# Performance work log

Hardware: AMD Instinct MI355X
Metric: run time of the kernel (lower is better)

Reference implementation:

```python
import jax, jax.numpy as jnp
import numpy as np

VOC, D, CPR, RELS = 2048, 128, 128, 7
B, DEPTH = 512, 4  # complete binary trees: 2**DEPTH leaves per tree


def setup_inputs() -> dict:
    key = jax.random.key(0)
    ks = jax.random.split(key, 13)
    s = lambda k, shape, fan: jax.random.normal(k, shape, jnp.float32) / np.sqrt(fan)
    return {
        "leaf_ids": jax.random.randint(ks[0], (B, 2, 2 ** DEPTH), 0, VOC),
        "Wv": s(ks[1], (D, VOC), VOC), "bv": jnp.zeros((D,), jnp.float32),
        "Wcps": s(ks[2], (D, 2 * D), 2 * D), "bcps": jnp.zeros((D,), jnp.float32),
        "Wcpst": s(ks[3], (D, D * D), D * D), "bcpst": jnp.zeros((D,), jnp.float32),
        "Wcpr": s(ks[4], (CPR, 2 * D), 2 * D), "bcpr": jnp.zeros((CPR,), jnp.float32),
        "Wcprt": s(ks[5], (CPR, D * D), D * D), "bcprt": jnp.zeros((CPR,), jnp.float32),
        "Wsm": s(ks[6], (RELS, CPR), CPR), "bsm": jnp.zeros((RELS,), jnp.float32),
    }


def reference(leaf_ids, Wv, bv, Wcps, bcps, Wcpst, bcpst, Wcpr, bcpr, Wcprt, bcprt, Wsm, bsm):
    d = Wv.shape[0]
    # leaf embedding: voc(one_hot(idx)) == Wv[:, idx] + bv  -> [B, 2, L, d]
    h = jnp.take(Wv.T, leaf_ids, axis=0) + bv
    # batched level-by-level tree composition (complete binary trees)
    while h.shape[2] > 1:
        l, r = h[:, :, 0::2, :], h[:, :, 1::2, :]
        lin = jnp.concatenate([l, r], axis=-1) @ Wcps.T + bcps
        kron = (l[..., :, None] * r[..., None, :]).reshape(l.shape[:-1] + (d * d,))
        h = jnp.tanh(lin + kron @ Wcpst.T + bcpst)
    lc, rc = h[:, 0, 0, :], h[:, 1, 0, :]  # [B, d] each
    cpr = jnp.concatenate([lc, rc], axis=-1) @ Wcpr.T + bcpr
    kron = (lc[:, :, None] * rc[:, None, :]).reshape(lc.shape[0], d * d)
    act = jax.nn.leaky_relu(cpr + kron @ Wcprt.T + bcprt, 0.01)
    logits = act @ Wsm.T + bsm
    return jax.nn.log_softmax(logits, axis=-1)  # [B, RELS]
```

## Files before the change

kernel.cpp:

```cpp
#include <hip/hip_runtime.h>
#include <hip/hip_bf16.h>
#include <hip/hip_fp16.h>

#define DD    128
#define VOCAB 2048
#define NRELS 7
#define NWF   (130 * 16384)

typedef _Float16 f16;
typedef __attribute__((ext_vector_type(8))) _Float16 f16x8;
typedef __attribute__((ext_vector_type(4))) float    f32x4;

__device__ __forceinline__ float lde(const void* p, size_t i, int bf) {
    if (bf) return (float)((const __hip_bfloat16*)p)[i];
    return ((const float*)p)[i];
}

__device__ __forceinline__ int detect_bf(const unsigned short* wv) {
    int sane = 0;
    #pragma unroll
    for (int i = 0; i < 64; ++i) {
        unsigned e = (wv[i] >> 7) & 0xFFu;
        sane += (e >= 90u && e <= 160u) ? 1 : 0;
    }
    return sane == 64;
}

__global__ void prep_all(const void* Wv, const void* bv,
                         const void* Wcps, const void* bcps,
                         const void* Wcpst, const void* bcpst,
                         const void* Wcpr, const void* bcpr,
                         const void* Wcprt, const void* bcprt,
                         const void* Wsm, const void* bsm,
                         f16* __restrict__ WvT, f16* __restrict__ Wext, f16* __restrict__ Wfin,
                         float* __restrict__ bias_lvl, float* __restrict__ bias_fin,
                         float* __restrict__ Wsm_f, float* __restrict__ bsm_f)
{
    const int bf = detect_bf((const unsigned short*)Wv);
    const int b = blockIdx.x;
    const int tid = threadIdx.x;

    if (b < 64) {
        __shared__ float tile[64][65];
        int vt = b >> 1, dt = b & 1;
        int tx = tid & 63, ty = tid >> 6;
        for (int yy = ty; yy < 64; yy += 4)
            tile[yy][tx] = lde(Wv, (size_t)(dt * 64 + yy) * VOCAB + vt * 64 + tx, bf);
        __syncthreads();
        for (int yy = ty; yy < 64; yy += 4) {
            int v = vt * 64 + yy, d = dt * 64 + tx;
            __builtin_nontemporal_store((f16)(tile[tx][yy] + lde(bv, d, bf)),
                                        &WvT[(size_t)v * DD + d]);
        }
        return;
    }
    if (b >= 2144) {
        if (tid < 128)      bias_lvl[tid] = lde(bcps, tid, bf) + lde(bcpst, tid, bf);
        else if (tid < 256) bias_fin[tid - 128] = lde(bcpr, tid - 128, bf) + lde(bcprt, tid - 128, bf);
        for (int o = tid; o < NRELS * DD; o += 256) Wsm_f[o] = lde(Wsm, o, bf);
        if (tid < NRELS) bsm_f[tid] = lde(bsm, tid, bf);
        return;
    }
    const int bb    = b - 64;
    const int which = bb / 1040;
    const int rem   = bb - which * 1040;
    const int i     = rem >> 3;
    const int n8    = rem & 7;
    const void* Wt = which ? (const void*)Wcprt : (const void*)Wcpst;
    const void* Ws = which ? (const void*)Wcpr  : (const void*)Wcps;
    f16* dst = which ? Wfin : Wext;

    __shared__ float tile[16 * 129];
    #pragma unroll
    for (int it = 0; it < 8; ++it) {
        int idx = it * 256 + tid;
        int rr = idx >> 7, c = idx & 127;
        float v = (i < 128) ? lde(Wt, (size_t)(n8 * 16 + rr) * 16384 + (size_t)i * 128 + c, bf)
                            : lde(Ws, (size_t)(n8 * 16 + rr) * 256 + (size_t)(i - 128) * 128 + c, bf);
        tile[rr * 129 + c] = v;
    }
    __syncthreads();
    f16* out = dst + (size_t)(i * 8 + n8) * 2048;
    #pragma unroll
    for (int it = 0; it < 8; ++it) {
        int o = it * 256 + tid;
        int t = o >> 9, ln = (o >> 3) & 63, e = o & 7;
        __builtin_nontemporal_store((f16)tile[(ln & 15) * 129 + t * 32 + ((ln >> 4) << 3) + e],
                                    &out[o]);
    }
}

template<int BI, int NW>
__launch_bounds__(NW * 64, 2)
__global__ void gemm_kernel(const f16* __restrict__ hin, const int* __restrict__ ids,
                            const f16* __restrict__ Wf,
                            f16* __restrict__ part, int Mrows, int S)
{
    __shared__ f16 Wb[4][8192];

    const int tid  = threadIdx.x;
    const int lane = tid & 63;
    const int wv   = tid >> 6;
    const int b    = blockIdx.x;
    const int nh   = (b >> 2) & 1;
    const int r    = ((b >> 3) << 2) | (b & 3);
    const int mb   = r / S;
    const int s    = r - mb * S;
    const int m0   = mb * (NW * 64);
    const int i0   = s * BI;
    const bool tail = (s == 1 || s == 2);
    const int itail = (s == 1) ? 128 : 129;

    const int mrow = lane & 15;
    const int q    = lane >> 4;
    const int wm   = wv * 64;

    f16x8 rf[4][4];
    int rowL[4];
    #pragma unroll
    for (int mt = 0; mt < 4; ++mt) {
        int p = m0 + wm + mt * 16 + mrow;
        int row = ids ? ids[2 * p + 1] : 2 * p + 1;
        rowL[mt] = ids ? ids[2 * p] : 2 * p;
        #pragma unroll
        for (int t = 0; t < 4; ++t)
            rf[mt][t] = *(const f16x8*)&hin[(size_t)row * DD + t * 32 + q * 8];
    }

    f16 lw[4][BI];
    #pragma unroll
    for (int mt = 0; mt < 4; ++mt) {
        const f16* src = &hin[(size_t)rowL[mt] * DD + i0];
        if constexpr (BI == 16) { *(f16x8*)&lw[mt][0] = *(const f16x8*)src;
                                  *(f16x8*)&lw[mt][8] = *(const f16x8*)(src + 8); }
        else if constexpr (BI == 8) { *(f16x8*)&lw[mt][0] = *(const f16x8*)src; }
        else if constexpr (BI == 4) { *(unsigned long long*)&lw[mt][0] = *(const unsigned long long*)src; }
        else if constexpr (BI == 2) { *(unsigned int*)&lw[mt][0] = *(const unsigned int*)src; }
        else { lw[mt][0] = src[0]; }
    }

    auto stage = [&](int i, int slot) {
        const f16* g = Wf + (size_t)i * 16384 + nh * 8192;
        #pragma unroll
        for (int k = 0; k < 16 / NW; ++k) {
            int j = k * NW + wv;
            const f16* gg = g + (size_t)(j * 64 + lane) * 8;
            f16* l = &Wb[slot][(size_t)(j * 64) * 8];
            __builtin_amdgcn_global_load_lds(
                (const __attribute__((address_space(1))) unsigned int*)gg,
                (__attribute__((address_space(3))) unsigned int*)l, 16, 0, 0);
        }
    };

    stage(i0, 0);
    if (BI > 1)       stage(i0 + 1, 1);
    else if (tail)    stage(itail, 1);
    __syncthreads();

    f32x4 acc[4][4] = {};

#define TSTEP(T, SLOT, KRON, LBV)                                                       \
    {                                                                                   \
        f16x8 wc[4];                                                                    \
        _Pragma("unroll")                                                               \
        for (int nt = 0; nt < 4; ++nt)                                                  \
            wc[nt] = *(const f16x8*)&Wb[SLOT][nt * 2048 + (T) * 512 + lane * 8];        \
        _Pragma("unroll")                                                               \
        for (int mt = 0; mt < 4; ++mt) {                                                \
            f16x8 a = (KRON) ? (LBV[mt] * rf[mt][T]) : rf[mt][T];                       \
            _Pragma("unroll")                                                           \
            for (int nt = 0; nt < 4; ++nt)                                              \
                acc[mt][nt] = __builtin_amdgcn_mfma_f32_16x16x32_f16(a, wc[nt], acc[mt][nt], 0, 0, 0); \
        }                                                                               \
    }

    #pragma unroll
    for (int ii = 0; ii < BI; ++ii) {
        if (ii + 2 < BI)                 stage(i0 + ii + 2, (ii + 2) & 3);
        else if (ii + 2 == BI && tail)   stage(itail, BI & 3);
        f16x8 lb[4];
        #pragma unroll
        for (int mt = 0; mt < 4; ++mt) {
            f16 v = lw[mt][ii];
            #pragma unroll
            for (int e = 0; e < 8; ++e) lb[mt][e] = v;
        }
        TSTEP(0, ii & 3, true, lb); TSTEP(1, ii & 3, true, lb);
        TSTEP(2, ii & 3, true, lb); TSTEP(3, ii & 3, true, lb);
        if (ii & 1) __syncthreads();
    }

    if (tail) {
        const int slot = (BI > 1) ? (BI & 3) : 1;
        if (s == 1) {
            #pragma unroll
            for (int mt = 0; mt < 4; ++mt)
                #pragma unroll
                for (int t = 0; t < 4; ++t)
                    rf[mt][t] = *(const f16x8*)&hin[(size_t)rowL[mt] * DD + t * 32 + q * 8];
        }
        f16x8 dummy[4];
        TSTEP(0, slot, false, dummy); TSTEP(1, slot, false, dummy);
        TSTEP(2, slot, false, dummy); TSTEP(3, slot, false, dummy);
    }
#undef TSTEP

    f16* pb = part + ((size_t)s * Mrows + m0) * DD + nh * 64;
    #pragma unroll
    for (int mt = 0; mt < 4; ++mt)
        #pragma unroll
        for (int nt = 0; nt < 4; ++nt) {
            int colg = nt * 16 + mrow;
            #pragma unroll
            for (int rr = 0; rr < 4; ++rr) {
                int rowl = wm + mt * 16 + q * 4 + rr;
                pb[(size_t)rowl * DD + colg] = (f16)acc[mt][nt][rr];
            }
        }
}

__global__ void epi_level(const f16* __restrict__ part, const float* __restrict__ bias,
                          f16* __restrict__ hout, int Mrows, int S)
{
    int idx = (blockIdx.x * 256 + threadIdx.x) * 8;
    size_t stride = (size_t)Mrows * DD;
    float sum[8] = {};
    for (int s2 = 0; s2 < S; ++s2) {
        f16x8 v = *(const f16x8*)&part[(size_t)s2 * stride + idx];
        #pragma unroll
        for (int e = 0; e < 8; ++e) sum[e] += (float)v[e];
    }
    int n = idx & 127;
    f16x8 o;
    #pragma unroll
    for (int e = 0; e < 8; ++e) o[e] = (f16)tanhf(sum[e] + bias[n + e]);
    *(f16x8*)&hout[idx] = o;
}

__global__ void fin_epi(const f16* __restrict__ part, const float* __restrict__ bias,
                        const float* __restrict__ Wsm_f, const float* __restrict__ bsm_f,
                        const unsigned short* __restrict__ wv_raw, void* __restrict__ outp, int S)
{
    int lane = threadIdx.x & 63;
    int wv = threadIdx.x >> 6;
    int p = blockIdx.x * 4 + wv;
    size_t stride = (size_t)512 * DD;
    const f16* base = part + (size_t)p * DD;
    float a0 = 0.f, a1 = 0.f;
    for (int s2 = 0; s2 < S; ++s2) {
        a0 += (float)base[(size_t)s2 * stride + lane];
        a1 += (float)base[(size_t)s2 * stride + 64 + lane];
    }
    a0 += bias[lane];      a1 += bias[64 + lane];
    a0 = (a0 > 0.f) ? a0 : 0.01f * a0;
    a1 = (a1 > 0.f) ? a1 : 0.01f * a1;
    float lg[NRELS];
    #pragma unroll
    for (int r = 0; r < NRELS; ++r) {
        float pr = a0 * Wsm_f[r * DD + lane] + a1 * Wsm_f[r * DD + 64 + lane];
        #pragma unroll
        for (int d = 1; d < 64; d <<= 1) pr += __shfl_xor(pr, d, 64);
        lg[r] = pr + bsm_f[r];
    }
    float mx = lg[0];
    #pragma unroll
    for (int r = 1; r < NRELS; ++r) mx = fmaxf(mx, lg[r]);
    float se = 0.f;
    #pragma unroll
    for (int r = 0; r < NRELS; ++r) se += expf(lg[r] - mx);
    float lse = logf(se) + mx;
    if (lane < NRELS) {
        float v = lg[lane] - lse;
        if (detect_bf(wv_raw)) ((__hip_bfloat16*)outp)[p * NRELS + lane] = __float2bfloat16(v);
        else                   ((float*)outp)[p * NRELS + lane] = v;
    }
}

extern "C" void kernel_launch(void* const* d_in, const int* in_sizes, int n_in,
                              void* d_out, int out_size, void* d_ws, size_t ws_size,
                              hipStream_t stream)
{
    const int* ids = (const int*)d_in[0];

    char* ws = (char*)d_ws;
    f16*   part     = (f16*)ws;
    f16*   h1       = (f16*)(ws + ((size_t)32 << 20));
    f16*   h2       = (f16*)(ws + ((size_t)34 << 20));
    f16*   h3       = (f16*)(ws + ((size_t)35 << 20));
    f16*   h4       = (f16*)(ws + ((size_t)35 << 20) + (512 << 10));
    f16*   WvT      = (f16*)(ws + ((size_t)36 << 20));
    f16*   Wext     = (f16*)(ws + ((size_t)36 << 20) + (512 << 10));
    f16*   Wfin     = Wext + (size_t)NWF;
    float* bias_lvl = (float*)(Wfin + (size_t)NWF);
    float* bias_fin = bias_lvl + 128;
    float* Wsm_f    = bias_fin + 128;
    float* bsm_f    = Wsm_f + NRELS * DD;

    if (ws_size < ((size_t)48 << 20)) return;

    prep_all<<<2145, 256, 0, stream>>>(d_in[1], d_in[2], d_in[3], d_in[4], d_in[5], d_in[6],
                                       d_in[7], d_in[8], d_in[9], d_in[10], d_in[11], d_in[12],
                                       WvT, Wext, Wfin, bias_lvl, bias_fin, Wsm_f, bsm_f);

    gemm_kernel<8, 8><<<512, 512, 0, stream>>>(WvT, ids, Wext, part, 8192, 16);
    epi_level<<<512, 256, 0, stream>>>(part, bias_lvl, h1, 8192, 16);
    gemm_kernel<4, 8><<<512, 512, 0, stream>>>(h1, nullptr, Wext, part, 4096, 32);
    epi_level<<<256, 256, 0, stream>>>(part, bias_lvl, h2, 4096, 32);
    gemm_kernel<4, 4><<<512, 256, 0, stream>>>(h2, nullptr, Wext, part, 2048, 32);
    epi_level<<<128, 256, 0, stream>>>(part, bias_lvl, h3, 2048, 32);
    gemm_kernel<4, 4><<<256, 256, 0, stream>>>(h3, nullptr, Wext, part, 1024, 32);
    epi_level<<<64, 256, 0, stream>>>(part, bias_lvl, h4, 1024, 32);
    gemm_kernel<2, 4><<<256, 256, 0, stream>>>(h4, nullptr, Wfin, part, 512, 64);
    fin_epi<<<128, 256, 0, stream>>>(part, bias_fin, Wsm_f, bsm_f,
                                     (const unsigned short*)d_in[1], d_out, 64);
}
```

Before: 274.3 us.

## Deepen GEMM weight prefetch pipeline with vmcnt waits and retune level launches

Restructures the GEMM main loop into a compile-time unrolled pipeline that prefetches three weight slices ahead into a four-slot LDS ring. It replaces __syncthreads with explicit s_waitcnt vmcnt counts plus raw s_barrier, and raises wave priority around the MFMA blocks. The tail slice is folded into the same schedule. The first two level launches switch to 4-wave blocks and fewer splits (BI 8, NW 4), trading grid shape for deeper per-block K work. The hand-counted vmcnt values risk races if other global loads are in flight.

```diff
diff --git a/kernel.cpp b/kernel.cpp
--- a/kernel.cpp
+++ b/kernel.cpp
@@ -24,6 +24,17 @@
         sane += (e >= 90u && e <= 160u) ? 1 : 0;
     }
     return sane == 64;
+}
+
+template<int N>
+__device__ __forceinline__ void wait_vmcnt() {
+    asm volatile("s_waitcnt vmcnt(%0)" :: "n"(N) : "memory");
+}
+template<int B> struct ic { static constexpr int value = B; };
+constexpr int wn_calc(int ii, int T) {
+    int tl = (ii + 3 < T - 1) ? (ii + 3) : (T - 1);
+    int n  = tl - (ii + 1);
+    return n < 0 ? 0 : n;
 }
 
 __global__ void prep_all(const void* Wv, const void* bv,
@@ -151,11 +162,6 @@
                 (__attribute__((address_space(3))) unsigned int*)l, 16, 0, 0);
         }
     };
-
-    stage(i0, 0);
-    if (BI > 1)       stage(i0 + 1, 1);
-    else if (tail)    stage(itail, 1);
-    __syncthreads();
 
     f32x4 acc[4][4] = {};
 
@@ -174,35 +180,64 @@
         }                                                                               \
     }
 
-    #pragma unroll
-    for (int ii = 0; ii < BI; ++ii) {
-        if (ii + 2 < BI)                 stage(i0 + ii + 2, (ii + 2) & 3);
-        else if (ii + 2 == BI && tail)   stage(itail, BI & 3);
-        f16x8 lb[4];
-        #pragma unroll
-        for (int mt = 0; mt < 4; ++mt) {
-            f16 v = lw[mt][ii];
-            #pragma unroll
-            for (int e = 0; e < 8; ++e) lb[mt][e] = v;
-        }
-        TSTEP(0, ii & 3, true, lb); TSTEP(1, ii & 3, true, lb);
-        TSTEP(2, ii & 3, true, lb); TSTEP(3, ii & 3, true, lb);
-        if (ii & 1) __syncthreads();
-    }
-
-    if (tail) {
-        const int slot = (BI > 1) ? (BI & 3) : 1;
-        if (s == 1) {
-            #pragma unroll
-            for (int mt = 0; mt < 4; ++mt)
-                #pragma unroll
-                for (int t = 0; t < 4; ++t)
-                    rf[mt][t] = *(const f16x8*)&hin[(size_t)rowL[mt] * DD + t * 32 + q * 8];
-        }
-        f16x8 dummy[4];
-        TSTEP(0, slot, false, dummy); TSTEP(1, slot, false, dummy);
-        TSTEP(2, slot, false, dummy); TSTEP(3, slot, false, dummy);
-    }
+    constexpr int L = 16 / NW;
+
+    auto run = [&](auto TC) {
+        constexpr int T = decltype(TC)::value;
+        auto dostage = [&](int t, int slot) {
+            stage((t < BI) ? (i0 + t) : itail, slot);
+        };
+        dostage(0, 0);
+        if constexpr (T > 1) dostage(1, 1);
+        if constexpr (T > 2) dostage(2, 2);
+        {
+            constexpr int tlp = (T - 1 < 2) ? (T - 1) : 2;
+            wait_vmcnt<tlp * L>();
+        }
+        __builtin_amdgcn_s_barrier();
+        __builtin_amdgcn_sched_barrier(0);
+
+#define GITER(II)                                                                       \
+        if constexpr (II < T) {                                                         \
+            if constexpr (II + 3 <= T - 1) dostage(II + 3, (II + 3) & 3);               \
+            wait_vmcnt<wn_calc(II, T) * L>();            \
+            if constexpr (II < BI) {                                                    \
+                f16x8 lb[4];                                                            \
+                _Pragma("unroll")                                                       \
+                for (int mt = 0; mt < 4; ++mt) {                                        \
+                    f16 v = lw[mt][II];                                                 \
+                    _Pragma("unroll")                                                   \
+                    for (int e = 0; e < 8; ++e) lb[mt][e] = v;                          \
+                }                                                                       \
+                __builtin_amdgcn_s_setprio(1);                                          \
+                TSTEP(0, II & 3, true, lb); TSTEP(1, II & 3, true, lb);                 \
+                TSTEP(2, II & 3, true, lb); TSTEP(3, II & 3, true, lb);                 \
+                __builtin_amdgcn_s_setprio(0);                                          \
+            } else {                               \
+                if (s == 1) {                 \
+                    _Pragma("unroll")                                                   \
+                    for (int mt = 0; mt < 4; ++mt)                                      \
+                        _Pragma("unroll")                                               \
+                        for (int t2 = 0; t2 < 4; ++t2)                                  \
+                            rf[mt][t2] = *(const f16x8*)&hin[(size_t)rowL[mt] * DD + t2 * 32 + q * 8]; \
+                }                                                                       \
+                f16x8 dummy[4];                                                         \
+                __builtin_amdgcn_s_setprio(1);                                          \
+                TSTEP(0, II & 3, false, dummy); TSTEP(1, II & 3, false, dummy);         \
+                TSTEP(2, II & 3, false, dummy); TSTEP(3, II & 3, false, dummy);         \
+                __builtin_amdgcn_s_setprio(0);                                          \
+            }                                                                           \
+            if constexpr (II + 1 < T) {                                                 \
+                __builtin_amdgcn_s_barrier();                                           \
+                __builtin_amdgcn_sched_barrier(0);                                      \
+            }                                                                           \
+        }
+        GITER(0) GITER(1) GITER(2) GITER(3) GITER(4)
+        GITER(5) GITER(6) GITER(7) GITER(8)
+#undef GITER
+    };
+    if (tail) run(ic<BI + 1>{});
+    else      run(ic<BI>{});
 #undef TSTEP
 
     f16* pb = part + ((size_t)s * Mrows + m0) * DD + nh * 64;
@@ -302,10 +337,10 @@
                                        d_in[7], d_in[8], d_in[9], d_in[10], d_in[11], d_in[12],
                                        WvT, Wext, Wfin, bias_lvl, bias_fin, Wsm_f, bsm_f);
 
-    gemm_kernel<8, 8><<<512, 512, 0, stream>>>(WvT, ids, Wext, part, 8192, 16);
+    gemm_kernel<8, 4><<<1024, 256, 0, stream>>>(WvT, ids, Wext, part, 8192, 16);
     epi_level<<<512, 256, 0, stream>>>(part, bias_lvl, h1, 8192, 16);
-    gemm_kernel<4, 8><<<512, 512, 0, stream>>>(h1, nullptr, Wext, part, 4096, 32);
-    epi_level<<<256, 256, 0, stream>>>(part, bias_lvl, h2, 4096, 32);
+    gemm_kernel<8, 4><<<512, 256, 0, stream>>>(h1, nullptr, Wext, part, 4096, 16);
+    epi_level<<<256, 256, 0, stream>>>(part, bias_lvl, h2, 4096, 16);
     gemm_kernel<4, 4><<<512, 256, 0, stream>>>(h2, nullptr, Wext, part, 2048, 32);
     epi_level<<<128, 256, 0, stream>>>(part, bias_lvl, h3, 2048, 32);
     gemm_kernel<4, 4><<<256, 256, 0, stream>>>(h3, nullptr, Wext, part, 1024, 32);
```

After: 388.2 us. 1.42x slower.
